# Performance work log

Hardware: AMD Instinct MI355X
Metric: run time of the kernel (lower is better)

## Reference

```python
import jax, jax.numpy as jnp
import numpy as np

N = 100000   # nodes
E = 1600000  # edges (avg degree 16)
H = 128      # hidden_dim
G = 256      # graphs in batch
IN = 2       # input feature dim (GCNConv(2, hidden_dim))


def setup_inputs() -> dict:
    key = jax.random.key(0)
    ks = jax.random.split(key, 12)
    def lin(k, fan_in, shape):
        # kaiming-uniform-ish init, scale irrelevant for correctness testing
        return jax.random.uniform(k, shape, jnp.float32, -1.0, 1.0) / np.sqrt(fan_in).astype(np.float32)
    return {
        "x": jax.random.normal(ks[0], (N, IN), jnp.float32),
        "edge_src": jax.random.randint(ks[1], (E,), 0, N, jnp.int32),
        "edge_dst": jax.random.randint(ks[2], (E,), 0, N, jnp.int32),
        "batch_ids": jnp.sort(jax.random.randint(ks[3], (N,), 0, G, jnp.int32)),
        "num_graphs": G,
        "W1": lin(ks[4], IN, (IN, H)), "b1": jnp.zeros((H,), jnp.float32),
        "W2": lin(ks[5], H, (H, H)),  "b2": jnp.zeros((H,), jnp.float32),
        "fc1_W": lin(ks[6], H, (H, H)), "fc1_b": lin(ks[7], H, (H,)),
        "fc2_W": lin(ks[8], H, (H, 1)), "fc2_b": lin(ks[9], H, (1,)),
    }


def gcn_layer(x, W, b, src, dst, n):
    # PyG GCNConv: add self-loops, symmetric deg^{-1/2} normalization,
    # linear transform, scatter-add aggregation, bias.
    h = x @ W                                                     # [N, H]
    deg = jax.ops.segment_sum(jnp.ones_like(src, jnp.float32), dst, num_segments=n) + 1.0  # +1 self-loop
    dinv = jax.lax.rsqrt(deg)                                     # [N]
    norm = dinv[src] * dinv[dst]                                  # [E]
    agg = jax.ops.segment_sum(h[src] * norm[:, None], dst, num_segments=n)  # [N, H]
    # self-loop contribution: deg_i^{-1/2} * deg_i^{-1/2} = 1/deg_i
    return agg + h * (1.0 / deg)[:, None] + b


def reference(x, edge_src, edge_dst, batch_ids, num_graphs,
              W1, b1, W2, b2, fc1_W, fc1_b, fc2_W, fc2_b):
    n = x.shape[0]
    h = jax.nn.relu(gcn_layer(x, W1, b1, edge_src, edge_dst, n))
    h = jax.nn.relu(gcn_layer(h, W2, b2, edge_src, edge_dst, n))
    # global_mean_pool
    sums = jax.ops.segment_sum(h, batch_ids, num_segments=num_graphs)            # [G, H]
    cnt = jax.ops.segment_sum(jnp.ones((n,), jnp.float32), batch_ids, num_segments=num_graphs)
    pooled = sums / jnp.maximum(cnt, 1.0)[:, None]
    h = jax.nn.relu(pooled @ fc1_W + fc1_b)
    return h @ fc2_W + fc2_b                                                     # [G, 1]
```

## Files before the change

### kernel.cpp

```cpp
#include <hip/hip_runtime.h>
#include <stdint.h>

#define HD 128
#define BSH 6
#define BNODES 64
#define PER 16

typedef float f32x4 __attribute__((ext_vector_type(4)));
typedef float f32x2 __attribute__((ext_vector_type(2)));
typedef short s16x8 __attribute__((ext_vector_type(8)));

static inline int idiv(int a, int b) { return (a + b - 1) / b; }

__device__ __forceinline__ unsigned short f2b(float f) {
  unsigned u = __float_as_uint(f);
  return (unsigned short)((u + 0x7fffu + ((u >> 16) & 1u)) >> 16);
}

__global__ void __launch_bounds__(256) k_cnt(const int* __restrict__ edst,
                                             int* __restrict__ btot,
                                             int E, int NB, int chunk) {
  __shared__ int hist[2048];
  int blk = blockIdx.x;
  for (int b = threadIdx.x; b < NB; b += 256) hist[b] = 0;
  __syncthreads();
  int s0 = blk * chunk, s1 = min(E, s0 + chunk);
  for (int k = s0 + threadIdx.x; k < s1; k += 256)
    atomicAdd(&hist[edst[k] >> BSH], 1);
  __syncthreads();
  for (int b = threadIdx.x; b < NB; b += 256) {
    int h = hist[b];
    if (h) atomicAdd(&btot[b], h);
  }
}

__global__ void __launch_bounds__(1024) k_bscan(const int* __restrict__ btot,
                                                int* __restrict__ bstart,
                                                int* __restrict__ gcur,
                                                int NB, int E) {
  __shared__ int sh[1024];
  int t = threadIdx.x;
  int a0 = (2 * t < NB) ? btot[2 * t] : 0;
  int a1 = (2 * t + 1 < NB) ? btot[2 * t + 1] : 0;
  int s = a0 + a1;
  sh[t] = s;
  __syncthreads();
  for (int off = 1; off < 1024; off <<= 1) {
    int add = (t >= off) ? sh[t - off] : 0;
    __syncthreads();
    sh[t] += add;
    __syncthreads();
  }
  int excl = sh[t] - s;
  if (2 * t < NB) { bstart[2 * t] = excl; gcur[2 * t] = excl; }
  if (2 * t + 1 < NB) { bstart[2 * t + 1] = excl + a0; gcur[2 * t + 1] = excl + a0; }
  if (t == 0) bstart[NB] = E;
}

__global__ void __launch_bounds__(256) k_binscatter2(const int* __restrict__ esrc,
                                                     const int* __restrict__ edst,
                                                     int* __restrict__ gcur,
                                                     unsigned* __restrict__ recs,
                                                     int E, int NB, int chunk) {
  __shared__ int hist[2048];
  int blk = blockIdx.x;
  for (int b = threadIdx.x; b < NB; b += 256) hist[b] = 0;
  __syncthreads();
  int s0 = blk * chunk, s1 = min(E, s0 + chunk);
  for (int k = s0 + threadIdx.x; k < s1; k += 256)
    atomicAdd(&hist[edst[k] >> BSH], 1);
  __syncthreads();
  for (int b = threadIdx.x; b < NB; b += 256) {
    int h = hist[b];
    hist[b] = h ? atomicAdd(&gcur[b], h) : 0;
  }
  __syncthreads();
  for (int k = s0 + threadIdx.x; k < s1; k += 256) {
    int d = edst[k], s = esrc[k];
    int b = d >> BSH;
    int pos = atomicAdd(&hist[b], 1);
    recs[pos] = ((unsigned)(d & (BNODES - 1)) << 26) | (unsigned)s;
  }
}

__global__ void __launch_bounds__(256) k_bucketsort(const unsigned* __restrict__ recs,
                                                    const int* __restrict__ bstart,
                                                    const float* __restrict__ x,
                                                    const int* __restrict__ bids,
                                                    unsigned* __restrict__ ssrc16,
                                                    int* __restrict__ row_start,
                                                    int* __restrict__ cnt,
                                                    float* __restrict__ dinv,
                                                    float2* __restrict__ xs,
                                                    int* __restrict__ gstart,
                                                    int NB, int N, int G) {
  __shared__ int count[BNODES], excl[BNODES], cur[BNODES];
  int b = blockIdx.x;
  int t = threadIdx.x;
  if (t < BNODES) count[t] = 0;
  __syncthreads();
  int rs = bstart[b];
  int re = bstart[b + 1];
  for (int k = rs + t; k < re; k += 256) atomicAdd(&count[recs[k] >> 26], 1);
  __syncthreads();
  if (t == 0) {
    int run = 0;
    for (int d = 0; d < BNODES; ++d) { excl[d] = run; run += count[d]; }
  }
  __syncthreads();
  if (t < BNODES) {
    int i = b * BNODES + t;
    if (i < N) {
      cnt[i] = count[t];
      row_start[i] = rs + excl[t];
      float di = rsqrtf((float)(count[t] + 1));
      dinv[i] = di;
      float2 xv = *(const float2*)&x[2 * i];
      xs[i] = make_float2(di * xv.x, di * xv.y);
      int g = bids[i];
      if (i == 0)
        for (int gg = 0; gg <= g; ++gg) gstart[gg] = 0;
      int gn = (i == N - 1) ? G : bids[i + 1];
      for (int gg = g + 1; gg <= gn; ++gg) gstart[gg] = i + 1;
    }
    cur[t] = excl[t];
  }
  __syncthreads();
  for (int k = rs + t; k < re; k += 256) {
    unsigned r = recs[k];
    int dl = r >> 26;
    int pos = rs + atomicAdd(&cur[dl], 1);
    ssrc16[pos] = (r & 0x03ffffffu) << 4;
  }
}

__global__ void k_aggx2(const int* __restrict__ row_start, const int* __restrict__ cnt,
                        const unsigned* __restrict__ ssrc16, const float2* __restrict__ xs,
                        const float* __restrict__ dinv, float4* __restrict__ td, int N) {
  int i = blockIdx.x * 256 + threadIdx.x;
  if (i >= N) return;
  int rs = row_start[i], re = rs + cnt[i];
  float a0 = 0.f, a1 = 0.f;
  int k = rs;
  for (; k + 1 < re; k += 2) {
    unsigned v0 = ssrc16[k] >> 4, v1 = ssrc16[k + 1] >> 4;
    float2 p0 = xs[v0], p1 = xs[v1];
    a0 += p0.x + p1.x; a1 += p0.y + p1.y;
  }
  if (k < re) {
    float2 p = xs[ssrc16[k] >> 4];
    a0 += p.x; a1 += p.y;
  }
  float2 self = xs[i];
  float di = dinv[i];
  td[i] = make_float4(di * (a0 + self.x), di * (a1 + self.y), di, 0.f);
}

__global__ void __launch_bounds__(256) k_aggh(
    const int* __restrict__ row_start, const int* __restrict__ cnt,
    const unsigned* __restrict__ ssrc16, const float4* __restrict__ td,
    const float* __restrict__ W1, const float* __restrict__ b1,
    unsigned* __restrict__ m_b, int N, int E) {
  __shared__ float4 sbuf[4][2][64];
  int wave = threadIdx.x >> 6;
  int lane = threadIdx.x & 63;
  int wid = blockIdx.x * 4 + wave;
  int i0 = wid * PER;
  if (i0 >= N) return;
  int nn = min(N - i0, PER);
  int j0 = lane * 2;
  f32x2 w0 = *(const f32x2*)&W1[j0];
  f32x2 w1 = *(const f32x2*)&W1[HD + j0];
  f32x2 bb = *(const f32x2*)&b1[j0];
  int mydeg = (lane < nn) ? cnt[i0 + lane] : 0;
  float4 mytd = (lane < nn) ? td[i0 + lane] : make_float4(0.f, 0.f, 0.f, 0.f);
  int mx = __float_as_int(mytd.x), my = __float_as_int(mytd.y), mz = __float_as_int(mytd.z);
  int rs0 = row_start[i0];
  int rsEnd = (i0 + nn < N) ? row_start[i0 + nn] : E;
  int total = rsEnd - rs0;
  int nb = (total + 63) >> 6;
  const char* tdc = (const char*)td;

  int node = 0;
  int rem = __builtin_amdgcn_readlane(mydeg, 0);
  f32x2 acc = {0.f, 0.f};

  auto finish = [&]() {
    float tx = __int_as_float(__builtin_amdgcn_readlane(mx, node));
    float ty = __int_as_float(__builtin_amdgcn_readlane(my, node));
    float tz = __int_as_float(__builtin_amdgcn_readlane(mz, node));
    f32x2 h = f32x2{ty, ty} * w1 + bb;
    h = f32x2{tx, tx} * w0 + h;
    h = __builtin_elementwise_max(h, f32x2{0.f, 0.f});
    f32x2 r = f32x2{tz, tz} * h + acc;
    m_b[((unsigned)(i0 + node) << 6) + lane] =
        ((unsigned)f2b(tz * r[1]) << 16) | f2b(tz * r[0]);
    acc = f32x2{0.f, 0.f};
    ++node;
    rem = (node < nn) ? __builtin_amdgcn_readlane(mydeg, node) : 0x7fffffff;
  };

  if (nb) {
    int eidx = rs0 + lane;
    unsigned off = (eidx < rsEnd) ? ssrc16[eidx] : 0u;
    float4 r0 = *(const float4*)(tdc + off);
    sbuf[wave][0][lane] = r0;
  }
  for (int b = 0; b < nb; ++b) {
    bool more = (b + 1 < nb);
    unsigned offn = 0u;
    float4 rn = make_float4(0.f, 0.f, 0.f, 0.f);
    if (more) {
      int eidx = rs0 + (b + 1) * 64 + lane;
      offn = (eidx < rsEnd) ? ssrc16[eidx] : 0u;
      rn = *(const float4*)(tdc + offn);
    }
    int cb = min(64, total - b * 64);
    const float4* buf = (const float4*)sbuf[wave][b & 1];
    int k = 0;
    while (k < cb) {
      while (rem == 0) finish();
      int take = min(rem, cb - k);
      for (int e = 0; e < take; ++e) {
        float4 t = buf[k + e];
        f32x2 h = f32x2{t.y, t.y} * w1 + bb;
        h = f32x2{t.x, t.x} * w0 + h;
        h = __builtin_elementwise_max(h, f32x2{0.f, 0.f});
        acc = f32x2{t.z, t.z} * h + acc;
      }
      k += take;
      rem -= take;
    }
    if (more) sbuf[wave][(b + 1) & 1][lane] = rn;
  }
  while (node < nn) finish();
}

__global__ void k_w2t(const float* __restrict__ W2, unsigned* __restrict__ w2f) {
  int f = blockIdx.x * 256 + threadIdx.x;
  if (f >= 2048) return;
  int c = f >> 8, s = (f >> 6) & 3, lane = f & 63;
  int col = c * 16 + (lane & 15);
  int kb = s * 32 + (lane >> 4) * 8;
  unsigned hi4[4], lo4[4];
#pragma unroll
  for (int j = 0; j < 4; ++j) {
    float w0 = W2[(kb + 2 * j) * HD + col];
    float w1 = W2[(kb + 2 * j + 1) * HD + col];
    unsigned short h0 = f2b(w0), h1 = f2b(w1);
    float r0 = w0 - __uint_as_float((unsigned)h0 << 16);
    float r1 = w1 - __uint_as_float((unsigned)h1 << 16);
    unsigned short l0 = f2b(r0), l1 = f2b(r1);
    hi4[j] = ((unsigned)h1 << 16) | h0;
    lo4[j] = ((unsigned)l1 << 16) | l0;
  }
  *(uint4*)&w2f[f * 4] = make_uint4(hi4[0], hi4[1], hi4[2], hi4[3]);
  *(uint4*)&w2f[8192 + f * 4] = make_uint4(lo4[0], lo4[1], lo4[2], lo4[3]);
}

__global__ void __launch_bounds__(256) k_t2pool(
    const unsigned* __restrict__ m_b, const unsigned* __restrict__ w2f,
    const float* __restrict__ b2, const int* __restrict__ gstart,
    const float* __restrict__ fc1W, const float* __restrict__ fc1b,
    const float* __restrict__ fc2W, const float* __restrict__ fc2b,
    float* __restrict__ out, int N, int G) {
  __shared__ unsigned W[16384];
  __shared__ float pool[16][HD];
  __shared__ float ps[HD];
  __shared__ float rsh[HD];
  int g = blockIdx.x;
  for (int u = threadIdx.x; u < 4096; u += 256)
    *(uint4*)&W[u * 4] = *(const uint4*)&w2f[u * 4];
  for (int u = threadIdx.x; u < 16 * HD; u += 256) ((float*)pool)[u] = 0.f;
  const int lane = threadIdx.x & 63;
  const int wave = threadIdx.x >> 6;
  const int col = lane & 15;
  const int kg = lane >> 4;
  float bb[8];
#pragma unroll
  for (int c = 0; c < 8; ++c) bb[c] = b2[c * 16 + col];
  int s0 = gstart[g], e0 = gstart[g + 1];
  int ntiles = (e0 - s0 + 15) >> 4;
  float pacc[8];
#pragma unroll
  for (int c = 0; c < 8; ++c) pacc[c] = 0.f;
  __syncthreads();
  for (int tile = wave; tile < ntiles; tile += 4) {
    int rbase = s0 + tile * 16;
    int arow = rbase + col;
    if (arow >= N) arow = N - 1;
    f32x4 acc[8];
#pragma unroll
    for (int c = 0; c < 8; ++c) acc[c] = f32x4{0.f, 0.f, 0.f, 0.f};
#pragma unroll
    for (int s = 0; s < 4; ++s) {
      uint4 av = *(const uint4*)&m_b[((size_t)arow << 6) + s * 16 + kg * 4];
      s16x8 A = *(s16x8*)&av;
#pragma unroll
      for (int c = 0; c < 8; ++c) {
        int f = (c * 4 + s) * 64 + lane;
        s16x8 Bh = *(s16x8*)&W[f * 4];
        s16x8 Bl = *(s16x8*)&W[8192 + f * 4];
        acc[c] = __builtin_amdgcn_mfma_f32_16x16x32_bf16(A, Bh, acc[c], 0, 0, 0);
        acc[c] = __builtin_amdgcn_mfma_f32_16x16x32_bf16(A, Bl, acc[c], 0, 0, 0);
      }
    }
    int orow = rbase + kg * 4;
#pragma unroll
    for (int c = 0; c < 8; ++c) {
#pragma unroll
      for (int r = 0; r < 4; ++r) {
        if (orow + r < e0) pacc[c] += fmaxf(acc[c][r] + bb[c], 0.f);
      }
    }
  }
#pragma unroll
  for (int c = 0; c < 8; ++c) pool[wave * 4 + kg][c * 16 + col] = pacc[c];
  __syncthreads();
  int j = threadIdx.x;
  if (j < HD) {
    float a = 0.f;
#pragma unroll
    for (int r = 0; r < 16; ++r) a += pool[r][j];
    float cg = (float)(e0 - s0);
    cg = cg < 1.f ? 1.f : cg;
    ps[j] = a / cg;
  }
  __syncthreads();
  if (j < HD) {
    float a = fc1b[j];
#pragma unroll 4
    for (int k = 0; k < HD; ++k) a = fmaf(ps[k], fc1W[k * HD + j], a);
    rsh[j] = fmaxf(a, 0.f) * fc2W[j];
  }
  __syncthreads();
  for (int off = 64; off > 0; off >>= 1) {
    if (j < off) rsh[j] += rsh[j + off];
    __syncthreads();
  }
  if (j == 0) out[g] = rsh[0] + fc2b[0];
}

extern "C" void kernel_launch(void* const* d_in, const int* in_sizes, int n_in,
                              void* d_out, int out_size, void* d_ws, size_t ws_size,
                              hipStream_t stream) {
  const float* x    = (const float*)d_in[0];
  const int* esrc   = (const int*)d_in[1];
  const int* edst   = (const int*)d_in[2];
  const int* bids   = (const int*)d_in[3];
  const float* W1   = (const float*)d_in[5];
  const float* b1   = (const float*)d_in[6];
  const float* W2   = (const float*)d_in[7];
  const float* b2   = (const float*)d_in[8];
  const float* fc1W = (const float*)d_in[9];
  const float* fc1b = (const float*)d_in[10];
  const float* fc2W = (const float*)d_in[11];
  const float* fc2b = (const float*)d_in[12];
  float* out = (float*)d_out;

  const int N = in_sizes[0] / 2;
  const int E = in_sizes[1];
  const int G = out_size;

  const int NB = idiv(N, BNODES);
  const int chunk = idiv(E, 256);

  char* w = (char*)d_ws;
  size_t o = 0;
  auto take = [&](size_t b) -> char* {
    char* p = w + o;
    o = (o + b + 255) & ~(size_t)255;
    return p;
  };
  int*      btot      = (int*)     take((size_t)NB * 4);
  size_t zero_bytes = o;
  int*      bstart    = (int*)     take((size_t)(NB + 1) * 4);
  int*      gcur      = (int*)     take((size_t)NB * 4);
  unsigned* recs      = (unsigned*)take((size_t)E * 4);
  unsigned* ssrc16    = (unsigned*)take((size_t)(E + 64) * 4);
  int*      cnt       = (int*)     take((size_t)N * 4);
  int*      row_start = (int*)     take((size_t)N * 4);
  float*    dinv      = (float*)   take((size_t)N * 4);
  float*    xs        = (float*)   take((size_t)N * 8);
  float*    td        = (float*)   take((size_t)N * 16);
  int*      gstart    = (int*)     take((size_t)(G + 1) * 4);
  unsigned* m_b       = (unsigned*)take((size_t)N * 64 * 4);
  unsigned* w2f       = (unsigned*)take(16384 * 4);

  hipMemsetAsync(d_ws, 0, zero_bytes, stream);

  k_w2t<<<8, 256, 0, stream>>>(W2, w2f);
  k_cnt<<<256, 256, 0, stream>>>(edst, btot, E, NB, chunk);
  k_bscan<<<1, 1024, 0, stream>>>(btot, bstart, gcur, NB, E);
  k_binscatter2<<<256, 256, 0, stream>>>(esrc, edst, gcur, recs, E, NB, chunk);
  k_bucketsort<<<NB, 256, 0, stream>>>(recs, bstart, x, bids, ssrc16, row_start,
                                       cnt, dinv, (float2*)xs, gstart, NB, N, G);
  k_aggx2<<<idiv(N, 256), 256, 0, stream>>>(row_start, cnt, ssrc16, (const float2*)xs,
                                            dinv, (float4*)td, N);
  int waves = idiv(N, PER);
  k_aggh<<<idiv(waves, 4), 256, 0, stream>>>(row_start, cnt, ssrc16, (const float4*)td,
                                             W1, b1, m_b, N, E);
  k_t2pool<<<G, 256, 0, stream>>>(m_b, w2f, b2, gstart, fc1W, fc1b, fc2W, fc2b, out, N, G);
}
```

Baseline: 147.4 us.

## Pad CSR rows to even length and process two edges per wave in k_aggh

The bucket sort now pads each node's edge list to an even length using a dummy source that points at a zeroed td[N] sentinel. This lets k_aggh split each wave into two half-waves that each handle one edge of a pair, with each lane computing 4 features; the halves are combined with a cross-half shuffle. The wave gathers up to 256 neighbor records into LDS in one pass instead of a double-buffered 64-edge streaming loop, and falls back to direct global loads when a group exceeds that. PER drops from 16 to 8 nodes per wave, which gives more waves and removes the irregular per-node finish logic, at the cost of padding work and more workspace.

Result: faster. 137.3 us (-6.9%).

```diff
diff --git a/kernel.cpp b/kernel.cpp
--- a/kernel.cpp
+++ b/kernel.cpp
@@ -4,7 +4,8 @@
 #define HD 128
 #define BSH 6
 #define BNODES 64
-#define PER 16
+#define PER 8
+#define SCAP 256
 
 typedef float f32x4 __attribute__((ext_vector_type(4)));
 typedef float f32x2 __attribute__((ext_vector_type(2)));
@@ -37,7 +38,8 @@
 __global__ void __launch_bounds__(1024) k_bscan(const int* __restrict__ btot,
                                                 int* __restrict__ bstart,
                                                 int* __restrict__ gcur,
-                                                int NB, int E) {
+                                                float4* __restrict__ td,
+                                                int NB, int E, int N) {
   __shared__ int sh[1024];
   int t = threadIdx.x;
   int a0 = (2 * t < NB) ? btot[2 * t] : 0;
@@ -54,7 +56,10 @@
   int excl = sh[t] - s;
   if (2 * t < NB) { bstart[2 * t] = excl; gcur[2 * t] = excl; }
   if (2 * t + 1 < NB) { bstart[2 * t + 1] = excl + a0; gcur[2 * t + 1] = excl + a0; }
-  if (t == 0) bstart[NB] = E;
+  if (t == 0) {
+    bstart[NB] = E;
+    td[N] = make_float4(0.f, 0.f, 0.f, 0.f);
+  }
 }
 
 __global__ void __launch_bounds__(256) k_binscatter2(const int* __restrict__ esrc,
@@ -101,18 +106,21 @@
   __syncthreads();
   int rs = bstart[b];
   int re = bstart[b + 1];
+  int base_p = rs + b * BNODES;
   for (int k = rs + t; k < re; k += 256) atomicAdd(&count[recs[k] >> 26], 1);
   __syncthreads();
   if (t == 0) {
     int run = 0;
-    for (int d = 0; d < BNODES; ++d) { excl[d] = run; run += count[d]; }
+    for (int d = 0; d < BNODES; ++d) { excl[d] = run; run += (count[d] + 1) & ~1; }
   }
   __syncthreads();
   if (t < BNODES) {
     int i = b * BNODES + t;
     if (i < N) {
       cnt[i] = count[t];
-      row_start[i] = rs + excl[t];
+      row_start[i] = base_p + excl[t];
+      if (count[t] & 1)
+        ssrc16[base_p + excl[t] + count[t]] = (unsigned)N << 4;
       float di = rsqrtf((float)(count[t] + 1));
       dinv[i] = di;
       float2 xv = *(const float2*)&x[2 * i];
@@ -129,7 +137,7 @@
   for (int k = rs + t; k < re; k += 256) {
     unsigned r = recs[k];
     int dl = r >> 26;
-    int pos = rs + atomicAdd(&cur[dl], 1);
+    int pos = base_p + atomicAdd(&cur[dl], 1);
     ssrc16[pos] = (r & 0x03ffffffu) << 4;
   }
 }
@@ -160,80 +168,80 @@
     const int* __restrict__ row_start, const int* __restrict__ cnt,
     const unsigned* __restrict__ ssrc16, const float4* __restrict__ td,
     const float* __restrict__ W1, const float* __restrict__ b1,
-    unsigned* __restrict__ m_b, int N, int E) {
-  __shared__ float4 sbuf[4][2][64];
+    unsigned* __restrict__ m_b, int N) {
+  __shared__ float4 sbuf[4][SCAP];
   int wave = threadIdx.x >> 6;
   int lane = threadIdx.x & 63;
   int wid = blockIdx.x * 4 + wave;
   int i0 = wid * PER;
   if (i0 >= N) return;
   int nn = min(N - i0, PER);
-  int j0 = lane * 2;
-  f32x2 w0 = *(const f32x2*)&W1[j0];
-  f32x2 w1 = *(const f32x2*)&W1[HD + j0];
-  f32x2 bb = *(const f32x2*)&b1[j0];
+  int hl = lane >> 5;
+  int fq = (lane & 31) * 4;
+  f32x4 w0 = *(const f32x4*)&W1[fq];
+  f32x4 w1 = *(const f32x4*)&W1[HD + fq];
+  f32x4 bb = *(const f32x4*)&b1[fq];
   int mydeg = (lane < nn) ? cnt[i0 + lane] : 0;
   float4 mytd = (lane < nn) ? td[i0 + lane] : make_float4(0.f, 0.f, 0.f, 0.f);
   int mx = __float_as_int(mytd.x), my = __float_as_int(mytd.y), mz = __float_as_int(mytd.z);
-  int rs0 = row_start[i0];
-  int rsEnd = (i0 + nn < N) ? row_start[i0 + nn] : E;
-  int total = rsEnd - rs0;
-  int nb = (total + 63) >> 6;
+  int mypad = (mydeg + 1) & ~1;
+  int total = 0;
+#pragma unroll
+  for (int u = 0; u < PER; ++u) total += __builtin_amdgcn_readlane(mypad, u);
+  int rs0 = __builtin_amdgcn_readfirstlane(row_start[i0]);
   const char* tdc = (const char*)td;
-
-  int node = 0;
-  int rem = __builtin_amdgcn_readlane(mydeg, 0);
-  f32x2 acc = {0.f, 0.f};
-
-  auto finish = [&]() {
+  bool staged = (total <= SCAP);
+  if (staged) {
+#pragma unroll
+    for (int w = 0; w < SCAP / 64; ++w) {
+      int sl = w * 64 + lane;
+      if (sl < total) {
+        unsigned off = ssrc16[rs0 + sl];
+        sbuf[wave][sl] = *(const float4*)(tdc + off);
+      }
+    }
+  }
+  int k = 0;
+  const f32x4 zero4 = {0.f, 0.f, 0.f, 0.f};
+  for (int node = 0; node < nn; ++node) {
+    int deg = __builtin_amdgcn_readlane(mydeg, node);
+    int np = (deg + 1) >> 1;
+    f32x4 acc = zero4;
+    if (staged) {
+#pragma unroll 2
+      for (int p = 0; p < np; ++p) {
+        float4 t = sbuf[wave][k + 2 * p + hl];
+        f32x4 h = f32x4{t.y, t.y, t.y, t.y} * w1 + bb;
+        h = f32x4{t.x, t.x, t.x, t.x} * w0 + h;
+        h = __builtin_elementwise_max(h, zero4);
+        acc = f32x4{t.z, t.z, t.z, t.z} * h + acc;
+      }
+    } else {
+      for (int p = 0; p < np; ++p) {
+        unsigned off = ssrc16[rs0 + k + 2 * p + hl];
+        float4 t = *(const float4*)(tdc + off);
+        f32x4 h = f32x4{t.y, t.y, t.y, t.y} * w1 + bb;
+        h = f32x4{t.x, t.x, t.x, t.x} * w0 + h;
+        h = __builtin_elementwise_max(h, zero4);
+        acc = f32x4{t.z, t.z, t.z, t.z} * h + acc;
+      }
+    }
+    k += np * 2;
+    f32x4 tot;
+#pragma unroll
+    for (int c = 0; c < 4; ++c) tot[c] = acc[c] + __shfl_xor(acc[c], 32);
     float tx = __int_as_float(__builtin_amdgcn_readlane(mx, node));
     float ty = __int_as_float(__builtin_amdgcn_readlane(my, node));
     float tz = __int_as_float(__builtin_amdgcn_readlane(mz, node));
-    f32x2 h = f32x2{ty, ty} * w1 + bb;
-    h = f32x2{tx, tx} * w0 + h;
-    h = __builtin_elementwise_max(h, f32x2{0.f, 0.f});
-    f32x2 r = f32x2{tz, tz} * h + acc;
-    m_b[((unsigned)(i0 + node) << 6) + lane] =
-        ((unsigned)f2b(tz * r[1]) << 16) | f2b(tz * r[0]);
-    acc = f32x2{0.f, 0.f};
-    ++node;
-    rem = (node < nn) ? __builtin_amdgcn_readlane(mydeg, node) : 0x7fffffff;
-  };
-
-  if (nb) {
-    int eidx = rs0 + lane;
-    unsigned off = (eidx < rsEnd) ? ssrc16[eidx] : 0u;
-    float4 r0 = *(const float4*)(tdc + off);
-    sbuf[wave][0][lane] = r0;
-  }
-  for (int b = 0; b < nb; ++b) {
-    bool more = (b + 1 < nb);
-    unsigned offn = 0u;
-    float4 rn = make_float4(0.f, 0.f, 0.f, 0.f);
-    if (more) {
-      int eidx = rs0 + (b + 1) * 64 + lane;
-      offn = (eidx < rsEnd) ? ssrc16[eidx] : 0u;
-      rn = *(const float4*)(tdc + offn);
-    }
-    int cb = min(64, total - b * 64);
-    const float4* buf = (const float4*)sbuf[wave][b & 1];
-    int k = 0;
-    while (k < cb) {
-      while (rem == 0) finish();
-      int take = min(rem, cb - k);
-      for (int e = 0; e < take; ++e) {
-        float4 t = buf[k + e];
-        f32x2 h = f32x2{t.y, t.y} * w1 + bb;
-        h = f32x2{t.x, t.x} * w0 + h;
-        h = __builtin_elementwise_max(h, f32x2{0.f, 0.f});
-        acc = f32x2{t.z, t.z} * h + acc;
-      }
-      k += take;
-      rem -= take;
-    }
-    if (more) sbuf[wave][(b + 1) & 1][lane] = rn;
-  }
-  while (node < nn) finish();
+    f32x4 h = f32x4{ty, ty, ty, ty} * w1 + bb;
+    h = f32x4{tx, tx, tx, tx} * w0 + h;
+    h = __builtin_elementwise_max(h, zero4);
+    f32x4 r = f32x4{tz, tz, tz, tz} * h + tot;
+    float v0 = (hl ? r[2] : r[0]) * tz;
+    float v1 = (hl ? r[3] : r[1]) * tz;
+    int j = hl ? (2 * (lane - 32) + 1) : (2 * lane);
+    m_b[(unsigned)(i0 + node) * 64 + j] = ((unsigned)f2b(v1) << 16) | f2b(v0);
+  }
 }
 
 __global__ void k_w2t(const float* __restrict__ W2, unsigned* __restrict__ w2f) {
@@ -377,12 +385,12 @@
   int*      bstart    = (int*)     take((size_t)(NB + 1) * 4);
   int*      gcur      = (int*)     take((size_t)NB * 4);
   unsigned* recs      = (unsigned*)take((size_t)E * 4);
-  unsigned* ssrc16    = (unsigned*)take((size_t)(E + 64) * 4);
+  unsigned* ssrc16    = (unsigned*)take((size_t)(E + (size_t)NB * BNODES + 128) * 4);
   int*      cnt       = (int*)     take((size_t)N * 4);
   int*      row_start = (int*)     take((size_t)N * 4);
   float*    dinv      = (float*)   take((size_t)N * 4);
   float*    xs        = (float*)   take((size_t)N * 8);
-  float*    td        = (float*)   take((size_t)N * 16);
+  float*    td        = (float*)   take((size_t)(N + 1) * 16);
   int*      gstart    = (int*)     take((size_t)(G + 1) * 4);
   unsigned* m_b       = (unsigned*)take((size_t)N * 64 * 4);
   unsigned* w2f       = (unsigned*)take(16384 * 4);
@@ -391,7 +399,7 @@
 
   k_w2t<<<8, 256, 0, stream>>>(W2, w2f);
   k_cnt<<<256, 256, 0, stream>>>(edst, btot, E, NB, chunk);
-  k_bscan<<<1, 1024, 0, stream>>>(btot, bstart, gcur, NB, E);
+  k_bscan<<<1, 1024, 0, stream>>>(btot, bstart, gcur, (float4*)td, NB, E, N);
   k_binscatter2<<<256, 256, 0, stream>>>(esrc, edst, gcur, recs, E, NB, chunk);
   k_bucketsort<<<NB, 256, 0, stream>>>(recs, bstart, x, bids, ssrc16, row_start,
                                        cnt, dinv, (float2*)xs, gstart, NB, N, G);
@@ -399,6 +407,6 @@
                                             dinv, (float4*)td, N);
   int waves = idiv(N, PER);
   k_aggh<<<idiv(waves, 4), 256, 0, stream>>>(row_start, cnt, ssrc16, (const float4*)td,
-                                             W1, b1, m_b, N, E);
+                                             W1, b1, m_b, N);
   k_t2pool<<<G, 256, 0, stream>>>(m_b, w2f, b2, gstart, fc1W, fc1b, fc2W, fc2b, out, N, G);
 }
```
